# Optimization experiments

Hardware: AMD Instinct MI355X
Metric: run time of the kernel (lower is better)

The kernel has to match this reference:

```python
import jax, jax.numpy as jnp
import numpy as np

K = 9
EPS = 1e-8
TAU2D = 2.0
BASE = jnp.array([[-1, -1], [0, -1], [1, -1], [-1, 0], [0, 0], [1, 0], [-1, 1], [0, 1], [1, 1]], dtype=jnp.float32)


def setup_inputs() -> dict:
    key = jax.random.key(0)
    ks = jax.random.split(key, 8)
    B, C, H, W, N = 4, 64, 256, 256, 16384
    hid, out_dim = 64, 1 + 1 + 2 * K + K
    feat_map = jax.random.normal(ks[0], (B, C, H, W), dtype=jnp.float32)
    coords_2d = jax.random.uniform(ks[1], (B, N, 2), dtype=jnp.float32) * 2.0 - 1.0  # normalized [-1,1]
    cell_2d = jax.random.uniform(ks[2], (B, N, 2), dtype=jnp.float32) * 0.02
    W1 = jax.random.normal(ks[3], (C + 4, hid), dtype=jnp.float32) * 0.05
    b1 = jnp.zeros((hid,), dtype=jnp.float32)
    Wr = jax.random.normal(ks[4], (hid, hid), dtype=jnp.float32) * 0.05
    br = jnp.zeros((hid,), dtype=jnp.float32)
    W2 = jax.random.normal(ks[5], (hid, out_dim), dtype=jnp.float32) * 0.05
    b2 = jnp.zeros((out_dim,), dtype=jnp.float32)
    return {"feat_map": feat_map, "coords_2d": coords_2d, "cell_2d": cell_2d,
            "W1": W1, "b1": b1, "Wr": Wr, "br": br, "W2": W2, "b2": b2}


def _grid_sample_1(feat, grid):
    # feat: (C,H,W), grid: (P,2) normalized coords, bilinear, border pad, align_corners=True
    C, H, W = feat.shape
    ix = jnp.clip((grid[:, 0] + 1.0) * 0.5 * (W - 1), 0.0, W - 1)
    iy = jnp.clip((grid[:, 1] + 1.0) * 0.5 * (H - 1), 0.0, H - 1)
    x0 = jnp.floor(ix)
    y0 = jnp.floor(iy)
    wx = ix - x0
    wy = iy - y0
    x0i = x0.astype(jnp.int32)
    y0i = y0.astype(jnp.int32)
    x1i = jnp.minimum(x0i + 1, W - 1)
    y1i = jnp.minimum(y0i + 1, H - 1)
    f00 = feat[:, y0i, x0i]  # (C,P)
    f01 = feat[:, y0i, x1i]
    f10 = feat[:, y1i, x0i]
    f11 = feat[:, y1i, x1i]
    return (f00 * (1 - wx) * (1 - wy) + f01 * wx * (1 - wy)
            + f10 * (1 - wx) * wy + f11 * wx * wy)  # (C,P)


_grid_sample = jax.vmap(_grid_sample_1)  # (B,C,H,W),(B,P,2)->(B,C,P)


def _leaky(x):
    return jnp.where(x >= 0, x, 0.2 * x)


def _forward(feat_map, coords_2d, cell_2d, W1, b1, Wr, br, W2, b2):
    B, C, H, W = feat_map.shape
    N = coords_2d.shape[1]
    # anchor features
    f_anchor = _grid_sample(feat_map, coords_2d).transpose(0, 2, 1)  # (B,N,C)
    router_in = jnp.concatenate([f_anchor, coords_2d, cell_2d], axis=-1)  # (B,N,C+4)
    h = _leaky(router_in @ W1 + b1)
    h = _leaky(h + (h @ Wr + br))  # residual block
    out = h @ W2 + b2  # (B,N,29)
    r_raw = out[..., 0:1]
    sigma_raw = out[..., 1:2]
    res_raw = out[..., 2:2 + 2 * K]
    gate_raw = out[..., 2 + 2 * K:2 + 3 * K]
    r = jnp.clip(jax.nn.softplus(r_raw) + 0.1, 0.1, 4.0)  # (B,N,1)
    sigma = jnp.clip(jax.nn.softplus(sigma_raw) + 0.5, 0.5, 6.0)  # (B,N,1)
    res = jnp.tanh(res_raw).reshape(B, N, K, 2) * 0.5
    offsets_pix = r[:, :, :, None] * BASE[None, None] + res  # (B,N,K,2)
    scale = jnp.array([2.0 / max(W - 1, 1), 2.0 / max(H - 1, 1)], dtype=jnp.float32)
    offsets_norm = offsets_pix * scale
    deform = coords_2d[:, :, None, :] + offsets_norm  # (B,N,K,2)
    f = _grid_sample(feat_map, deform.reshape(B, N * K, 2))  # (B,C,N*K)
    f = f.reshape(B, C, N, K).transpose(0, 2, 3, 1)  # (B,N,K,C)
    d2 = offsets_pix[..., 0] ** 2 + offsets_pix[..., 1] ** 2  # (B,N,K)
    sig_eff = sigma * TAU2D  # (B,N,1)
    w_geo = jnp.exp(-0.5 * d2 / (sig_eff ** 2 + EPS))
    gate = jax.nn.sigmoid(gate_raw)
    w = w_geo * gate
    w = w / (jnp.sum(w, axis=-1, keepdims=True) + EPS)
    out_feat = jnp.einsum('bnkc,bnk->bnc', f, w)
    return out_feat


def reference(feat_map, coords_2d, cell_2d, W1, b1, Wr, br, W2, b2):
    return _forward(feat_map, coords_2d, cell_2d, W1, b1, Wr, br, W2, b2)
```

## Files before the change

kernel.cpp:

```cpp
#include <hip/hip_runtime.h>

#define K_TAPS 9
#define CC 64
#define HH 256
#define WW 256
#define BB 4
#define NN 16384
#define NPTS (BB * NN)
#define SCLX (2.0f / 255.0f)
#define SCLY (2.0f / 255.0f)
#define PRM_STRIDE 32
#define AS 68

__device__ __forceinline__ float softplus_f(float x) {
    return fmaxf(x, 0.0f) + log1pf(expf(-fabsf(x)));
}
__device__ __forceinline__ float leaky_f(float x) { return x >= 0.0f ? x : 0.2f * x; }
__device__ __forceinline__ float clampf(float x, float lo, float hi) {
    return fminf(fmaxf(x, lo), hi);
}
__device__ __forceinline__ float bf2f(unsigned short u) {
    union { unsigned int i; float f; } v;
    v.i = (unsigned int)u << 16;
    return v.f;
}
__device__ __forceinline__ unsigned short f2bf(float f) {
    union { float f; unsigned int i; } v;
    v.f = f;
    unsigned int r = (v.i + 0x7FFFu + ((v.i >> 16) & 1u)) >> 16;
    return (unsigned short)r;
}

__global__ void __launch_bounds__(256) transpose_kernel(const float* __restrict__ feat,
                                                        unsigned int* __restrict__ featB) {
    __shared__ float tile[64][65];
    int b = blockIdx.y;
    int p0 = blockIdx.x * 64;
    int tp = threadIdx.x & 63;
    int tq = threadIdx.x >> 6;
    const float* fb = feat + (size_t)b * CC * HH * WW;
#pragma unroll
    for (int i = 0; i < 16; ++i) {
        int c = tq * 16 + i;
        tile[c][tp] = fb[(size_t)c * (HH * WW) + p0 + tp];
    }
    __syncthreads();
    unsigned int* ob = featB + ((size_t)b * (HH * WW) + p0) * 32;
    int c2 = threadIdx.x & 31;
    int psub = threadIdx.x >> 5;
#pragma unroll
    for (int i = 0; i < 8; ++i) {
        int p = i * 8 + psub;
        unsigned int lo = f2bf(tile[2 * c2][p]);
        unsigned int hi = f2bf(tile[2 * c2 + 1][p]);
        ob[(size_t)p * 32 + c2] = lo | (hi << 16);
    }
}

__device__ __forceinline__ float4 bilin4_bf(const unsigned short* __restrict__ base, float gx,
                                            float gy, int c4) {
    float ix = clampf((gx + 1.0f) * 0.5f * 255.0f, 0.0f, 255.0f);
    float iy = clampf((gy + 1.0f) * 0.5f * 255.0f, 0.0f, 255.0f);
    float x0f = floorf(ix), y0f = floorf(iy);
    float wx = ix - x0f, wy = iy - y0f;
    int x0 = (int)x0f, y0 = (int)y0f;
    int x1 = min(x0 + 1, 255), y1 = min(y0 + 1, 255);
    const ushort4 u00 = *(const ushort4*)(base + (size_t)(((y0 << 8) + x0) * 64) + c4 * 4);
    const ushort4 u01 = *(const ushort4*)(base + (size_t)(((y0 << 8) + x1) * 64) + c4 * 4);
    const ushort4 u10 = *(const ushort4*)(base + (size_t)(((y1 << 8) + x0) * 64) + c4 * 4);
    const ushort4 u11 = *(const ushort4*)(base + (size_t)(((y1 << 8) + x1) * 64) + c4 * 4);
    float w00 = (1.0f - wx) * (1.0f - wy), w01 = wx * (1.0f - wy);
    float w10 = (1.0f - wx) * wy, w11 = wx * wy;
    float4 v;
    v.x = bf2f(u00.x) * w00 + bf2f(u01.x) * w01 + bf2f(u10.x) * w10 + bf2f(u11.x) * w11;
    v.y = bf2f(u00.y) * w00 + bf2f(u01.y) * w01 + bf2f(u10.y) * w10 + bf2f(u11.y) * w11;
    v.z = bf2f(u00.z) * w00 + bf2f(u01.z) * w01 + bf2f(u10.z) * w10 + bf2f(u11.z) * w11;
    v.w = bf2f(u00.w) * w00 + bf2f(u01.w) * w01 + bf2f(u10.w) * w01 * 0.0f +
          bf2f(u10.w) * w10 + bf2f(u11.w) * w11;
    v.w = bf2f(u00.w) * w00 + bf2f(u01.w) * w01 + bf2f(u10.w) * w10 + bf2f(u11.w) * w11;
    return v;
}

__global__ void __launch_bounds__(256) mlp_kernel(const unsigned short* __restrict__ featB,
                                                  const float* __restrict__ coords,
                                                  const float* __restrict__ cell,
                                                  const float* __restrict__ W1,
                                                  const float* __restrict__ b1,
                                                  const float* __restrict__ Wr,
                                                  const float* __restrict__ br,
                                                  const float* __restrict__ W2,
                                                  const float* __restrict__ b2,
                                                  float* __restrict__ prm) {
    __shared__ __align__(16) float act[68 * AS];
    __shared__ __align__(16) float wbuf[68 * 64];
    float4* wbuf4 = (float4*)wbuf;

    const int t = threadIdx.x;
    const int q = t & 15;
    const int pgrp = t >> 4;
    const int blk0 = blockIdx.x * 64;

    {
        const float4* w1g = (const float4*)W1;
#pragma unroll
        for (int idx = t; idx < 1088; idx += 256) wbuf4[idx] = w1g[idx];
    }

    {
        const int pt = t & 63;
        const int wvi = t >> 6;
        const int pg = blk0 + pt;
        const int bb = pg >> 14;
        const float gx = coords[2 * pg], gy = coords[2 * pg + 1];
        float ix = clampf((gx + 1.0f) * 0.5f * 255.0f, 0.0f, 255.0f);
        float iy = clampf((gy + 1.0f) * 0.5f * 255.0f, 0.0f, 255.0f);
        float x0f = floorf(ix), y0f = floorf(iy);
        float wx = ix - x0f, wy = iy - y0f;
        int x0 = (int)x0f, y0 = (int)y0f;
        int x1 = min(x0 + 1, 255), y1 = min(y0 + 1, 255);
        const unsigned short* base = featB + (size_t)bb * (HH * WW) * 64;
        size_t i00 = (size_t)(((y0 << 8) + x0) * 64), i01 = (size_t)(((y0 << 8) + x1) * 64);
        size_t i10 = (size_t)(((y1 << 8) + x0) * 64), i11 = (size_t)(((y1 << 8) + x1) * 64);
        float w00 = (1.0f - wx) * (1.0f - wy), w01 = wx * (1.0f - wy);
        float w10 = (1.0f - wx) * wy, w11 = wx * wy;
#pragma unroll
        for (int g = 0; g < 4; ++g) {
            int qq = 4 * g + wvi;
            ushort4 u00 = *(const ushort4*)(base + i00 + qq * 4);
            ushort4 u01 = *(const ushort4*)(base + i01 + qq * 4);
            ushort4 u10 = *(const ushort4*)(base + i10 + qq * 4);
            ushort4 u11 = *(const ushort4*)(base + i11 + qq * 4);
            act[(4 * qq + 0) * AS + pt] =
                bf2f(u00.x) * w00 + bf2f(u01.x) * w01 + bf2f(u10.x) * w10 + bf2f(u11.x) * w11;
            act[(4 * qq + 1) * AS + pt] =
                bf2f(u00.y) * w00 + bf2f(u01.y) * w01 + bf2f(u10.y) * w10 + bf2f(u11.y) * w11;
            act[(4 * qq + 2) * AS + pt] =
                bf2f(u00.z) * w00 + bf2f(u01.z) * w01 + bf2f(u10.z) * w10 + bf2f(u11.z) * w11;
            act[(4 * qq + 3) * AS + pt] =
                bf2f(u00.w) * w00 + bf2f(u01.w) * w01 + bf2f(u10.w) * w10 + bf2f(u11.w) * w11;
        }
        if (wvi == 0) {
            act[64 * AS + pt] = gx;
            act[65 * AS + pt] = gy;
            act[66 * AS + pt] = cell[2 * pg];
            act[67 * AS + pt] = cell[2 * pg + 1];
        }
    }
    __syncthreads();

    float hres[4][4];
    {
        float acc[4][4];
        float4 b4 = ((const float4*)b1)[q];
        float bj[4] = {b4.x, b4.y, b4.z, b4.w};
#pragma unroll
        for (int j = 0; j < 4; ++j)
#pragma unroll
            for (int p = 0; p < 4; ++p) acc[j][p] = bj[j];
#pragma unroll 4
        for (int i = 0; i < 68; ++i) {
            float4 av = *(const float4*)&act[i * AS + 4 * pgrp];
            float4 wv4 = *(const float4*)&wbuf[i * 64 + 4 * q];
            float a[4] = {av.x, av.y, av.z, av.w};
            float wj[4] = {wv4.x, wv4.y, wv4.z, wv4.w};
#pragma unroll
            for (int j = 0; j < 4; ++j)
#pragma unroll
                for (int p = 0; p < 4; ++p) acc[j][p] = fmaf(a[p], wj[j], acc[j][p]);
        }
#pragma unroll
        for (int j = 0; j < 4; ++j)
#pragma unroll
            for (int p = 0; p < 4; ++p) hres[j][p] = leaky_f(acc[j][p]);
    }
    __syncthreads();

#pragma unroll
    for (int j = 0; j < 4; ++j)
        *(float4*)&act[(4 * q + j) * AS + 4 * pgrp] =
            make_float4(hres[j][0], hres[j][1], hres[j][2], hres[j][3]);
    {
        const float4* wrg = (const float4*)Wr;
#pragma unroll
        for (int idx = t; idx < 1024; idx += 256) wbuf4[idx] = wrg[idx];
    }
    __syncthreads();

    float h2[4][4];
    {
        float4 b4 = ((const float4*)br)[q];
        float bj[4] = {b4.x, b4.y, b4.z, b4.w};
#pragma unroll
        for (int j = 0; j < 4; ++j)
#pragma unroll
            for (int p = 0; p < 4; ++p) h2[j][p] = bj[j];
#pragma unroll 4
        for (int i = 0; i < 64; ++i) {
            float4 av = *(const float4*)&act[i * AS + 4 * pgrp];
            float4 wv4 = *(const float4*)&wbuf[i * 64 + 4 * q];
            float a[4] = {av.x, av.y, av.z, av.w};
            float wj[4] = {wv4.x, wv4.y, wv4.z, wv4.w};
#pragma unroll
            for (int j = 0; j < 4; ++j)
#pragma unroll
                for (int p = 0; p < 4; ++p) h2[j][p] = fmaf(a[p], wj[j], h2[j][p]);
        }
#pragma unroll
        for (int j = 0; j < 4; ++j)
#pragma unroll
            for (int p = 0; p < 4; ++p) h2[j][p] = leaky_f(hres[j][p] + h2[j][p]);
    }
    __syncthreads();

#pragma unroll
    for (int j = 0; j < 4; ++j)
        *(float4*)&act[(4 * q + j) * AS + 4 * pgrp] =
            make_float4(h2[j][0], h2[j][1], h2[j][2], h2[j][3]);
    {
        const float4* w2g = (const float4*)W2;
#pragma unroll
        for (int idx = t; idx < 464; idx += 256) wbuf4[idx] = w2g[idx];
    }
    __syncthreads();

    float* sot = wbuf + 2048;

    {
        const int j0 = 2 * q, j1 = 2 * q + 1;
        const int jj0 = min(j0, 28), jj1 = min(j1, 28);
        float o0[4], o1[4];
        float bb0 = b2[jj0], bb1 = b2[jj1];
#pragma unroll
        for (int p = 0; p < 4; ++p) {
            o0[p] = bb0;
            o1[p] = bb1;
        }
#pragma unroll 4
        for (int i = 0; i < 64; ++i) {
            float4 av = *(const float4*)&act[i * AS + 4 * pgrp];
            float a[4] = {av.x, av.y, av.z, av.w};
            float w0 = wbuf[i * 29 + jj0], w1 = wbuf[i * 29 + jj1];
#pragma unroll
            for (int p = 0; p < 4; ++p) {
                o0[p] = fmaf(a[p], w0, o0[p]);
                o1[p] = fmaf(a[p], w1, o1[p]);
            }
        }
#pragma unroll
        for (int p = 0; p < 4; ++p) {
            int pt = 4 * pgrp + p;
            if (j0 < 29) sot[pt * 30 + j0] = o0[p];
            if (j1 < 29) sot[pt * 30 + j1] = o1[p];
        }
    }
    __syncthreads();

    {
        const int pt = t >> 2, sub = t & 3;
        const int pg = blk0 + pt;
        const float* so = sot + pt * 30;
        float gx = coords[2 * pg], gy = coords[2 * pg + 1];
        float r = clampf(softplus_f(so[0]) + 0.1f, 0.1f, 4.0f);
        float sg = clampf(softplus_f(so[1]) + 0.5f, 0.5f, 6.0f);
        float se = sg * 2.0f;
        float inv2 = -0.5f / (se * se + 1e-8f);
        float sx[3], sy[3], wv[3];
        float s = 0.0f;
#pragma unroll
        for (int ii = 0; ii < 3; ++ii) {
            int kr = 4 * ii + sub;
            int k = kr < 9 ? kr : 0;
            float bx = (float)(k % 3 - 1);
            float by = (float)(k / 3 - 1);
            float ox = fmaf(r, bx, tanhf(so[2 + 2 * k]) * 0.5f);
            float oy = fmaf(r, by, tanhf(so[3 + 2 * k]) * 0.5f);
            float d2 = ox * ox + oy * oy;
            float wgeo = expf(d2 * inv2);
            float gate = 1.0f / (1.0f + expf(-so[20 + k]));
            float w = (kr < 9) ? wgeo * gate : 0.0f;
            wv[ii] = w;
            s += w;
            sx[ii] = fmaf(ox, SCLX, gx);
            sy[ii] = fmaf(oy, SCLY, gy);
        }
        s += __shfl_xor(s, 1, 64);
        s += __shfl_xor(s, 2, 64);
        float inv = 1.0f / (s + 1e-8f);
        float* pp = prm + (size_t)pg * PRM_STRIDE;
#pragma unroll
        for (int ii = 0; ii < 3; ++ii) {
            int kr = 4 * ii + sub;
            if (kr < 9) {
                pp[3 * kr + 0] = sx[ii];
                pp[3 * kr + 1] = sy[ii];
                pp[3 * kr + 2] = wv[ii] * inv;
            }
        }
    }
}

__global__ void __launch_bounds__(256) gather_kernel(const unsigned short* __restrict__ featB,
                                                     const float* __restrict__ prm,
                                                     float4* __restrict__ out4) {
    int tid = blockIdx.x * 256 + threadIdx.x;
    int c4 = tid & 15;
    int p = tid >> 4;
    int bb = p >> 14;
    const unsigned short* base = featB + (size_t)bb * (HH * WW) * 64;
    const float* pp = prm + (size_t)p * PRM_STRIDE;
    float4 acc = make_float4(0.0f, 0.0f, 0.0f, 0.0f);
#pragma unroll 3
    for (int k = 0; k < K_TAPS; ++k) {
        float sx = pp[3 * k + 0];
        float sy = pp[3 * k + 1];
        float wk = pp[3 * k + 2];
        float4 v = bilin4_bf(base, sx, sy, c4);
        acc.x = fmaf(v.x, wk, acc.x);
        acc.y = fmaf(v.y, wk, acc.y);
        acc.z = fmaf(v.z, wk, acc.z);
        acc.w = fmaf(v.w, wk, acc.w);
    }
    out4[(size_t)p * 16 + c4] = acc;
}

__device__ __forceinline__ float bilin_chw(const float* __restrict__ feat, int b, int lane,
                                           float gx, float gy) {
    float ix = clampf((gx + 1.0f) * 0.5f * 255.0f, 0.0f, 255.0f);
    float iy = clampf((gy + 1.0f) * 0.5f * 255.0f, 0.0f, 255.0f);
    float x0f = floorf(ix), y0f = floorf(iy);
    float wx = ix - x0f, wy = iy - y0f;
    int x0 = (int)x0f, y0 = (int)y0f;
    int x1 = min(x0 + 1, 255), y1 = min(y0 + 1, 255);
    const float* base = feat + ((size_t)b * CC + lane) * (HH * WW);
    float f00 = base[(y0 << 8) + x0];
    float f01 = base[(y0 << 8) + x1];
    float f10 = base[(y1 << 8) + x0];
    float f11 = base[(y1 << 8) + x1];
    float omx = 1.0f - wx, omy = 1.0f - wy;
    return (f00 * omx + f01 * wx) * omy + (f10 * omx + f11 * wx) * wy;
}

__global__ void __launch_bounds__(256) fallback_kernel(const float* __restrict__ feat,
                                                       const float* __restrict__ coords,
                                                       const float* __restrict__ cell,
                                                       const float* __restrict__ W1,
                                                       const float* __restrict__ b1,
                                                       const float* __restrict__ Wr,
                                                       const float* __restrict__ br,
                                                       const float* __restrict__ W2,
                                                       const float* __restrict__ b2,
                                                       float* __restrict__ out) {
    int lane = threadIdx.x & 63;
    int wave = threadIdx.x >> 6;
    int pidx = blockIdx.x * 4 + wave;
    if (pidx >= NPTS) return;
    int b = pidx >> 14;
    float gx = coords[(size_t)pidx * 2 + 0];
    float gy = coords[(size_t)pidx * 2 + 1];
    float cx = cell[(size_t)pidx * 2 + 0];
    float cy = cell[(size_t)pidx * 2 + 1];
    float fa = bilin_chw(feat, b, lane, gx, gy);
    float h = b1[lane];
#pragma unroll
    for (int i = 0; i < 64; ++i) {
        float a = __shfl(fa, i, 64);
        h = fmaf(a, W1[i * 64 + lane], h);
    }
    h = fmaf(gx, W1[64 * 64 + lane], h);
    h = fmaf(gy, W1[65 * 64 + lane], h);
    h = fmaf(cx, W1[66 * 64 + lane], h);
    h = fmaf(cy, W1[67 * 64 + lane], h);
    h = leaky_f(h);
    float h2 = br[lane];
#pragma unroll
    for (int i = 0; i < 64; ++i) {
        float a = __shfl(h, i, 64);
        h2 = fmaf(a, Wr[i * 64 + lane], h2);
    }
    h2 = leaky_f(h + h2);
    int j = lane < 29 ? lane : 0;
    float o = b2[j];
#pragma unroll
    for (int i = 0; i < 64; ++i) {
        float a = __shfl(h2, i, 64);
        o = fmaf(a, W2[i * 29 + j], o);
    }
    int kk = lane < K_TAPS ? lane : 0;
    float r_raw = __shfl(o, 0, 64);
    float s_raw = __shfl(o, 1, 64);
    float rx_raw = __shfl(o, 2 + 2 * kk, 64);
    float ry_raw = __shfl(o, 3 + 2 * kk, 64);
    float g_raw = __shfl(o, 20 + kk, 64);
    float r = clampf(softplus_f(r_raw) + 0.1f, 0.1f, 4.0f);
    float sg = clampf(softplus_f(s_raw) + 0.5f, 0.5f, 6.0f);
    float bx = (float)(kk % 3 - 1);
    float by = (float)(kk / 3 - 1);
    float offx = fmaf(r, bx, tanhf(rx_raw) * 0.5f);
    float offy = fmaf(r, by, tanhf(ry_raw) * 0.5f);
    float d2 = offx * offx + offy * offy;
    float se = sg * 2.0f;
    float wgeo = expf(-0.5f * d2 / (se * se + 1e-8f));
    float gate = 1.0f / (1.0f + expf(-g_raw));
    float w = wgeo * gate;
    float wv = (lane < K_TAPS) ? w : 0.0f;
#pragma unroll
    for (int m = 32; m >= 1; m >>= 1) wv += __shfl_xor(wv, m, 64);
    float wn = w / (wv + 1e-8f);
    float acc = 0.0f;
#pragma unroll
    for (int k = 0; k < K_TAPS; ++k) {
        float ox = __shfl(offx, k, 64) * SCLX;
        float oy = __shfl(offy, k, 64) * SCLY;
        float wk2 = __shfl(wn, k, 64);
        float fv = bilin_chw(feat, b, lane, gx + ox, gy + oy);
        acc = fmaf(fv, wk2, acc);
    }
    out[(size_t)pidx * CC + lane] = acc;
}

extern "C" void kernel_launch(void* const* d_in, const int* in_sizes, int n_in,
                              void* d_out, int out_size, void* d_ws, size_t ws_size,
                              hipStream_t stream) {
    const float* feat = (const float*)d_in[0];
    const float* coords = (const float*)d_in[1];
    const float* cell = (const float*)d_in[2];
    const float* W1 = (const float*)d_in[3];
    const float* b1 = (const float*)d_in[4];
    const float* Wr = (const float*)d_in[5];
    const float* br = (const float*)d_in[6];
    const float* W2 = (const float*)d_in[7];
    const float* b2 = (const float*)d_in[8];
    float* out = (float*)d_out;

    const size_t needT = (size_t)BB * HH * WW * CC * sizeof(unsigned short);
    const size_t needP = (size_t)NPTS * PRM_STRIDE * sizeof(float);

    if (ws_size >= needT + needP) {
        unsigned short* featB = (unsigned short*)d_ws;
        float* prm = (float*)((char*)d_ws + needT);
        dim3 tg((HH * WW) / 64, BB);
        transpose_kernel<<<tg, 256, 0, stream>>>(feat, (unsigned int*)featB);
        mlp_kernel<<<NPTS / 64, 256, 0, stream>>>(featB, coords, cell, W1, b1, Wr, br, W2, b2,
                                                  prm);
        gather_kernel<<<(NPTS * 16) / 256, 256, 0, stream>>>(featB, prm, (float4*)out);
    } else {
        fallback_kernel<<<NPTS / 4, 256, 0, stream>>>(feat, coords, cell, W1, b1, Wr, br, W2,
                                                      b2, out);
    }
}
```

Measured before the change: 81.90 us.

## Fuse MLP and deformable gather kernels, keep tap params in shared memory

Merges the router MLP kernel and the gather kernel into one kernel. Per-point sample positions and weights now stay in shared memory (reusing the weight buffer) instead of being written to and reread from a global workspace, which also removes one launch. It also issues the W1 weight loads and the anchor bilinear loads into registers before the shared-memory stores, so their latencies overlap. The cost is that each thread now does four gather tasks serially after the MLP, and the extra register arrays may lower occupancy.

```diff
diff --git a/kernel.cpp b/kernel.cpp
--- a/kernel.cpp
+++ b/kernel.cpp
@@ -75,22 +75,20 @@
     v.x = bf2f(u00.x) * w00 + bf2f(u01.x) * w01 + bf2f(u10.x) * w10 + bf2f(u11.x) * w11;
     v.y = bf2f(u00.y) * w00 + bf2f(u01.y) * w01 + bf2f(u10.y) * w10 + bf2f(u11.y) * w11;
     v.z = bf2f(u00.z) * w00 + bf2f(u01.z) * w01 + bf2f(u10.z) * w10 + bf2f(u11.z) * w11;
-    v.w = bf2f(u00.w) * w00 + bf2f(u01.w) * w01 + bf2f(u10.w) * w01 * 0.0f +
-          bf2f(u10.w) * w10 + bf2f(u11.w) * w11;
     v.w = bf2f(u00.w) * w00 + bf2f(u01.w) * w01 + bf2f(u10.w) * w10 + bf2f(u11.w) * w11;
     return v;
 }
 
-__global__ void __launch_bounds__(256) mlp_kernel(const unsigned short* __restrict__ featB,
-                                                  const float* __restrict__ coords,
-                                                  const float* __restrict__ cell,
-                                                  const float* __restrict__ W1,
-                                                  const float* __restrict__ b1,
-                                                  const float* __restrict__ Wr,
-                                                  const float* __restrict__ br,
-                                                  const float* __restrict__ W2,
-                                                  const float* __restrict__ b2,
-                                                  float* __restrict__ prm) {
+__global__ void __launch_bounds__(256) fused_kernel(const unsigned short* __restrict__ featB,
+                                                    const float* __restrict__ coords,
+                                                    const float* __restrict__ cell,
+                                                    const float* __restrict__ W1,
+                                                    const float* __restrict__ b1,
+                                                    const float* __restrict__ Wr,
+                                                    const float* __restrict__ br,
+                                                    const float* __restrict__ W2,
+                                                    const float* __restrict__ b2,
+                                                    float4* __restrict__ out4) {
     __shared__ __align__(16) float act[68 * AS];
     __shared__ __align__(16) float wbuf[68 * 64];
     float4* wbuf4 = (float4*)wbuf;
@@ -99,12 +97,6 @@
     const int q = t & 15;
     const int pgrp = t >> 4;
     const int blk0 = blockIdx.x * 64;
-
-    {
-        const float4* w1g = (const float4*)W1;
-#pragma unroll
-        for (int idx = t; idx < 1088; idx += 256) wbuf4[idx] = w1g[idx];
-    }
 
     {
         const int pt = t & 63;
@@ -112,6 +104,15 @@
         const int pg = blk0 + pt;
         const int bb = pg >> 14;
         const float gx = coords[2 * pg], gy = coords[2 * pg + 1];
+
+        const float4* w1g = (const float4*)W1;
+        float4 w1r0 = w1g[t];
+        float4 w1r1 = w1g[t + 256];
+        float4 w1r2 = w1g[t + 512];
+        float4 w1r3 = w1g[t + 768];
+        float4 w1x;
+        if (t < 64) w1x = w1g[1024 + t];
+
         float ix = clampf((gx + 1.0f) * 0.5f * 255.0f, 0.0f, 255.0f);
         float iy = clampf((gy + 1.0f) * 0.5f * 255.0f, 0.0f, 255.0f);
         float x0f = floorf(ix), y0f = floorf(iy);
@@ -121,23 +122,35 @@
         const unsigned short* base = featB + (size_t)bb * (HH * WW) * 64;
         size_t i00 = (size_t)(((y0 << 8) + x0) * 64), i01 = (size_t)(((y0 << 8) + x1) * 64);
         size_t i10 = (size_t)(((y1 << 8) + x0) * 64), i11 = (size_t)(((y1 << 8) + x1) * 64);
+        ushort4 u00[4], u01[4], u10[4], u11[4];
+#pragma unroll
+        for (int g = 0; g < 4; ++g) {
+            int qq = 4 * g + wvi;
+            u00[g] = *(const ushort4*)(base + i00 + qq * 4);
+            u01[g] = *(const ushort4*)(base + i01 + qq * 4);
+            u10[g] = *(const ushort4*)(base + i10 + qq * 4);
+            u11[g] = *(const ushort4*)(base + i11 + qq * 4);
+        }
+
+        wbuf4[t] = w1r0;
+        wbuf4[t + 256] = w1r1;
+        wbuf4[t + 512] = w1r2;
+        wbuf4[t + 768] = w1r3;
+        if (t < 64) wbuf4[1024 + t] = w1x;
+
         float w00 = (1.0f - wx) * (1.0f - wy), w01 = wx * (1.0f - wy);
         float w10 = (1.0f - wx) * wy, w11 = wx * wy;
 #pragma unroll
         for (int g = 0; g < 4; ++g) {
             int qq = 4 * g + wvi;
-            ushort4 u00 = *(const ushort4*)(base + i00 + qq * 4);
-            ushort4 u01 = *(const ushort4*)(base + i01 + qq * 4);
-            ushort4 u10 = *(const ushort4*)(base + i10 + qq * 4);
-            ushort4 u11 = *(const ushort4*)(base + i11 + qq * 4);
-            act[(4 * qq + 0) * AS + pt] =
-                bf2f(u00.x) * w00 + bf2f(u01.x) * w01 + bf2f(u10.x) * w10 + bf2f(u11.x) * w11;
-            act[(4 * qq + 1) * AS + pt] =
-                bf2f(u00.y) * w00 + bf2f(u01.y) * w01 + bf2f(u10.y) * w10 + bf2f(u11.y) * w11;
-            act[(4 * qq + 2) * AS + pt] =
-                bf2f(u00.z) * w00 + bf2f(u01.z) * w01 + bf2f(u10.z) * w10 + bf2f(u11.z) * w11;
-            act[(4 * qq + 3) * AS + pt] =
-                bf2f(u00.w) * w00 + bf2f(u01.w) * w01 + bf2f(u10.w) * w10 + bf2f(u11.w) * w11;
+            act[(4 * qq + 0) * AS + pt] = bf2f(u00[g].x) * w00 + bf2f(u01[g].x) * w01 +
+                                          bf2f(u10[g].x) * w10 + bf2f(u11[g].x) * w11;
+            act[(4 * qq + 1) * AS + pt] = bf2f(u00[g].y) * w00 + bf2f(u01[g].y) * w01 +
+                                          bf2f(u10[g].y) * w10 + bf2f(u11[g].y) * w11;
+            act[(4 * qq + 2) * AS + pt] = bf2f(u00[g].z) * w00 + bf2f(u01[g].z) * w01 +
+                                          bf2f(u10[g].z) * w10 + bf2f(u11[g].z) * w11;
+            act[(4 * qq + 3) * AS + pt] = bf2f(u00[g].w) * w00 + bf2f(u01[g].w) * w01 +
+                                          bf2f(u10[g].w) * w10 + bf2f(u11[g].w) * w11;
         }
         if (wvi == 0) {
             act[64 * AS + pt] = gx;
@@ -224,6 +237,7 @@
     __syncthreads();
 
     float* sot = wbuf + 2048;
+    float* prm = wbuf;
 
     {
         const int j0 = 2 * q, j1 = 2 * q + 1;
@@ -286,7 +300,7 @@
         s += __shfl_xor(s, 1, 64);
         s += __shfl_xor(s, 2, 64);
         float inv = 1.0f / (s + 1e-8f);
-        float* pp = prm + (size_t)pg * PRM_STRIDE;
+        float* pp = prm + pt * 28;
 #pragma unroll
         for (int ii = 0; ii < 3; ++ii) {
             int kr = 4 * ii + sub;
@@ -297,30 +311,31 @@
             }
         }
     }
-}
-
-__global__ void __launch_bounds__(256) gather_kernel(const unsigned short* __restrict__ featB,
-                                                     const float* __restrict__ prm,
-                                                     float4* __restrict__ out4) {
-    int tid = blockIdx.x * 256 + threadIdx.x;
-    int c4 = tid & 15;
-    int p = tid >> 4;
-    int bb = p >> 14;
-    const unsigned short* base = featB + (size_t)bb * (HH * WW) * 64;
-    const float* pp = prm + (size_t)p * PRM_STRIDE;
-    float4 acc = make_float4(0.0f, 0.0f, 0.0f, 0.0f);
+    __syncthreads();
+
+#pragma unroll
+    for (int g = 0; g < 4; ++g) {
+        int task = g * 256 + t;
+        int c4 = task & 15;
+        int pt = task >> 4;
+        int pg = blk0 + pt;
+        int bb = pg >> 14;
+        const unsigned short* base = featB + (size_t)bb * (HH * WW) * 64;
+        const float* pp = prm + pt * 28;
+        float4 acc = make_float4(0.0f, 0.0f, 0.0f, 0.0f);
 #pragma unroll 3
-    for (int k = 0; k < K_TAPS; ++k) {
-        float sx = pp[3 * k + 0];
-        float sy = pp[3 * k + 1];
-        float wk = pp[3 * k + 2];
-        float4 v = bilin4_bf(base, sx, sy, c4);
-        acc.x = fmaf(v.x, wk, acc.x);
-        acc.y = fmaf(v.y, wk, acc.y);
-        acc.z = fmaf(v.z, wk, acc.z);
-        acc.w = fmaf(v.w, wk, acc.w);
-    }
-    out4[(size_t)p * 16 + c4] = acc;
+        for (int k = 0; k < K_TAPS; ++k) {
+            float sx = pp[3 * k + 0];
+            float sy = pp[3 * k + 1];
+            float wk = pp[3 * k + 2];
+            float4 v = bilin4_bf(base, sx, sy, c4);
+            acc.x = fmaf(v.x, wk, acc.x);
+            acc.y = fmaf(v.y, wk, acc.y);
+            acc.z = fmaf(v.z, wk, acc.z);
+            acc.w = fmaf(v.w, wk, acc.w);
+        }
+        out4[(size_t)pg * 16 + c4] = acc;
+    }
 }
 
 __device__ __forceinline__ float bilin_chw(const float* __restrict__ feat, int b, int lane,
@@ -433,16 +448,13 @@
     float* out = (float*)d_out;
 
     const size_t needT = (size_t)BB * HH * WW * CC * sizeof(unsigned short);
-    const size_t needP = (size_t)NPTS * PRM_STRIDE * sizeof(float);
-
-    if (ws_size >= needT + needP) {
+
+    if (ws_size >= needT) {
         unsigned short* featB = (unsigned short*)d_ws;
-        float* prm = (float*)((char*)d_ws + needT);
         dim3 tg((HH * WW) / 64, BB);
         transpose_kernel<<<tg, 256, 0, stream>>>(feat, (unsigned int*)featB);
-        mlp_kernel<<<NPTS / 64, 256, 0, stream>>>(featB, coords, cell, W1, b1, Wr, br, W2, b2,
-                                                  prm);
-        gather_kernel<<<(NPTS * 16) / 256, 256, 0, stream>>>(featB, prm, (float4*)out);
+        fused_kernel<<<NPTS / 64, 256, 0, stream>>>(featB, coords, cell, W1, b1, Wr, br, W2,
+                                                    b2, (float4*)out);
     } else {
         fallback_kernel<<<NPTS / 4, 256, 0, stream>>>(feat, coords, cell, W1, b1, Wr, br, W2,
                                                       b2, out);
```

Result: faster. 73.64 us (-10.1%).
